# Kernel tuning notes

Hardware: AMD Instinct MI355X
Metric: run time of the kernel (lower is better)

Reference implementation:

```python
import jax, jax.numpy as jnp
import numpy as np

N_NODES = 40000
N_EDGES = 1280000
D_FEAT = 1024
HIDDEN = 64
N_CLASSES = 40


def gcn_conv(x, edge_index, W, b):
    # PyG GCNConv: linear transform, add self-loops, symmetric deg^{-1/2} normalization, scatter-add
    n = x.shape[0]
    h = x @ W  # [N, out]
    loop = jnp.arange(n, dtype=edge_index.dtype)
    row = jnp.concatenate([edge_index[0], loop])  # source
    col = jnp.concatenate([edge_index[1], loop])  # target
    deg = jax.ops.segment_sum(jnp.ones_like(col, dtype=x.dtype), col, num_segments=n)
    dinv = jnp.where(deg > 0, jax.lax.rsqrt(deg), 0.0).astype(x.dtype)
    norm = dinv[row] * dinv[col]  # [E+N]
    msg = h[row] * norm[:, None]
    out = jax.ops.segment_sum(msg, col, num_segments=n)
    return out + b


def setup_inputs() -> dict:
    key = jax.random.key(0)
    k1, k2, k3, k4 = jax.random.split(key, 4)
    x = jax.random.normal(k1, (N_NODES, D_FEAT), dtype=jnp.float32)
    edge_index = jax.random.randint(k2, (2, N_EDGES), 0, N_NODES, dtype=jnp.int32)
    W1 = jax.random.normal(k3, (D_FEAT, HIDDEN), dtype=jnp.float32) * (1.0 / np.sqrt(D_FEAT))
    b1 = jnp.zeros((HIDDEN,), dtype=jnp.float32)
    W2 = jax.random.normal(k4, (HIDDEN, N_CLASSES), dtype=jnp.float32) * (1.0 / np.sqrt(HIDDEN))
    b2 = jnp.zeros((N_CLASSES,), dtype=jnp.float32)
    return {"x": x, "edge_index": edge_index, "W1": W1, "b1": b1, "W2": W2, "b2": b2}


def reference(x, edge_index, W1, b1, W2, b2):
    h = gcn_conv(x, edge_index, W1, b1)
    h = jax.nn.relu(h)
    # F.dropout(training=False) -> identity in eval mode
    h = gcn_conv(h, edge_index, W2, b2)
    return jax.nn.log_softmax(h, axis=1)
```

## Files before the change

kernel.cpp:

```cpp
#include <hip/hip_runtime.h>
#include <hip/hip_bf16.h>
#include <math.h>

#define N_NODES 40000
#define N_EDGES 1280000
#define D_FEAT 1024
#define HIDDEN 64
#define N_CLASSES 40
#define NB 157
#define CHUNK 8192

typedef _Float16 f16x8 __attribute__((ext_vector_type(8)));
typedef _Float16 f16x2 __attribute__((ext_vector_type(2)));
typedef float f32x4 __attribute__((ext_vector_type(4)));


#define HIST_BLOCKS 313
#define CONV_BLOCKS 256

__global__ __launch_bounds__(256) void k_pre(const int* __restrict__ col,
                                             int* __restrict__ btot,
                                             const float* __restrict__ W,
                                             _Float16* __restrict__ Wt) {
    __shared__ int h[NB];
    int tid = threadIdx.x;
    if (blockIdx.x < HIST_BLOCKS) {
        if (tid < NB) h[tid] = 0;
        __syncthreads();
        int e0 = blockIdx.x * 4096;
        int e1 = min(e0 + 4096, N_EDGES);
        for (int e = e0 + tid; e < e1; e += 256)
            atomicAdd(&h[col[e] >> 8], 1);
        __syncthreads();
        if (tid < NB && h[tid]) atomicAdd(&btot[tid], h[tid]);
    } else {
        int i = (blockIdx.x - HIST_BLOCKS) * 256 + tid;
        int n = i & 63, k = i >> 6;
        Wt[n * D_FEAT + k] = (_Float16)W[k * HIDDEN + n];
    }
}


__global__ __launch_bounds__(256) void k_bucketscan(const int* __restrict__ btot,
                                                    int* __restrict__ bucketBase,
                                                    int* __restrict__ bucketCursor) {
    __shared__ int s[256];
    int tid = threadIdx.x;
    int v = (tid < NB) ? btot[tid] : 0;
    s[tid] = v;
    __syncthreads();
#pragma unroll
    for (int d = 1; d < 256; d <<= 1) {
        int t = (tid >= d) ? s[tid - d] : 0;
        __syncthreads();
        s[tid] += t;
        __syncthreads();
    }
    int excl = s[tid] - v;
    if (tid < NB) { bucketBase[tid] = excl; bucketCursor[tid] = excl; }
    if (tid == 0) bucketBase[NB] = N_EDGES;
}


__global__ __launch_bounds__(256) void k_binscatter(const int* __restrict__ row,
                                                    const int* __restrict__ col,
                                                    int* __restrict__ bucketCursor,
                                                    uint2* __restrict__ sedge) {
    __shared__ int hist[NB];
    __shared__ int chunkBase[NB];
    __shared__ int cur[NB];
    int tid = threadIdx.x;
    int e0 = blockIdx.x * CHUNK;
    int e1 = min(e0 + CHUNK, N_EDGES);
    if (tid < NB) { hist[tid] = 0; cur[tid] = 0; }
    __syncthreads();
    for (int e = e0 + tid; e < e1; e += 256)
        atomicAdd(&hist[col[e] >> 8], 1);
    __syncthreads();
    if (tid < NB)
        chunkBase[tid] = hist[tid] ? atomicAdd(&bucketCursor[tid], hist[tid]) : 0;
    __syncthreads();
    for (int e = e0 + tid; e < e1; e += 256) {
        int c = col[e];
        int b = c >> 8;
        int p = atomicAdd(&cur[b], 1);
        sedge[chunkBase[b] + p] = make_uint2((unsigned)row[e], (unsigned)c);
    }
}


__global__ __launch_bounds__(256) void k_bucketsort(const uint2* __restrict__ sedge,
                                                    const int* __restrict__ bucketBase,
                                                    int* __restrict__ off,
                                                    float* __restrict__ dinv,
                                                    int* __restrict__ sorted) {
    __shared__ int hist[256];
    __shared__ int s[256];
    __shared__ int cur[256];
    int tid = threadIdx.x;
    int b = blockIdx.x;
    int base = bucketBase[b], end = bucketBase[b + 1];
    int col0 = b << 8;
    int ncol = min(256, N_NODES - col0);
    hist[tid] = 0;
    __syncthreads();
    for (int i = base + tid; i < end; i += 256)
        atomicAdd(&hist[sedge[i].y & 255], 1);
    __syncthreads();
    int v = hist[tid];
    s[tid] = v;
    __syncthreads();
#pragma unroll
    for (int d = 1; d < 256; d <<= 1) {
        int t = (tid >= d) ? s[tid - d] : 0;
        __syncthreads();
        s[tid] += t;
        __syncthreads();
    }
    int excl = s[tid] - v;
    cur[tid] = excl;
    if (tid < ncol) {
        off[col0 + tid] = base + excl;
        dinv[col0 + tid] = rsqrtf((float)(v + 1));
    }
    if (b == NB - 1 && tid == 0) off[N_NODES] = N_EDGES;
    __syncthreads();
    for (int i = base + tid; i < end; i += 256) {
        uint2 e = sedge[i];
        int p = atomicAdd(&cur[e.y & 255], 1);
        sorted[base + p] = (int)e.x;
    }
}


#define LDA 72
#define LDB 72

__global__ __launch_bounds__(256) void k_gemm1(const float* __restrict__ X,
                                               const _Float16* __restrict__ Wt,
                                               const float* __restrict__ dinv,
                                               _Float16* __restrict__ out) {
    __shared__ _Float16 As[64 * LDA];
    __shared__ _Float16 Bs[64 * LDB];
    const int tid = threadIdx.x;
    const int wave = tid >> 6, lane = tid & 63;
    const int row0 = blockIdx.x * 64;
    const int m0 = wave * 16;
    const int lr = lane & 15, quad = lane >> 4;

    const int ar = tid >> 2;
    const int ak = (tid & 3) * 16;

    f32x4 acc0 = {0.f,0.f,0.f,0.f}, acc1 = {0.f,0.f,0.f,0.f};
    f32x4 acc2 = {0.f,0.f,0.f,0.f}, acc3 = {0.f,0.f,0.f,0.f};

    for (int k0 = 0; k0 < D_FEAT; k0 += 64) {
        const float* xp = &X[(row0 + ar) * D_FEAT + k0 + ak];
        float4 v0 = *(const float4*)(xp + 0);
        float4 v1 = *(const float4*)(xp + 4);
        float4 v2 = *(const float4*)(xp + 8);
        float4 v3 = *(const float4*)(xp + 12);
        f16x8 p0 = {(_Float16)v0.x,(_Float16)v0.y,(_Float16)v0.z,(_Float16)v0.w,
                    (_Float16)v1.x,(_Float16)v1.y,(_Float16)v1.z,(_Float16)v1.w};
        f16x8 p1 = {(_Float16)v2.x,(_Float16)v2.y,(_Float16)v2.z,(_Float16)v2.w,
                    (_Float16)v3.x,(_Float16)v3.y,(_Float16)v3.z,(_Float16)v3.w};
        *(f16x8*)&As[ar * LDA + ak]     = p0;
        *(f16x8*)&As[ar * LDA + ak + 8] = p1;
        const uint4* wp = (const uint4*)&Wt[ar * D_FEAT + k0 + ak];
        uint4 w0 = wp[0], w1 = wp[1];
        *(uint4*)&Bs[ar * LDB + ak]     = w0;
        *(uint4*)&Bs[ar * LDB + ak + 8] = w1;
        __syncthreads();
#pragma unroll
        for (int kk = 0; kk < 64; kk += 32) {
            f16x8 a  = *(f16x8*)&As[(m0 + lr) * LDA + kk + quad * 8];
            f16x8 b0 = *(f16x8*)&Bs[( 0 + lr) * LDB + kk + quad * 8];
            f16x8 b1 = *(f16x8*)&Bs[(16 + lr) * LDB + kk + quad * 8];
            f16x8 b2 = *(f16x8*)&Bs[(32 + lr) * LDB + kk + quad * 8];
            f16x8 b3 = *(f16x8*)&Bs[(48 + lr) * LDB + kk + quad * 8];
            acc0 = __builtin_amdgcn_mfma_f32_16x16x32_f16(a, b0, acc0, 0, 0, 0);
            acc1 = __builtin_amdgcn_mfma_f32_16x16x32_f16(a, b1, acc1, 0, 0, 0);
            acc2 = __builtin_amdgcn_mfma_f32_16x16x32_f16(a, b2, acc2, 0, 0, 0);
            acc3 = __builtin_amdgcn_mfma_f32_16x16x32_f16(a, b3, acc3, 0, 0, 0);
        }
        __syncthreads();
    }

#pragma unroll
    for (int r = 0; r < 4; ++r) {
        int m = row0 + m0 + quad * 4 + r;
        float dv = dinv[m];
        out[m * HIDDEN +  0 + lr] = (_Float16)(acc0[r] * dv);
        out[m * HIDDEN + 16 + lr] = (_Float16)(acc1[r] * dv);
        out[m * HIDDEN + 32 + lr] = (_Float16)(acc2[r] * dv);
        out[m * HIDDEN + 48 + lr] = (_Float16)(acc3[r] * dv);
    }
}


__global__ __launch_bounds__(256) void k_g1g2(const int* __restrict__ off,
                                              const int* __restrict__ sorted,
                                              const _Float16* __restrict__ hs,
                                              const float* __restrict__ dinv,
                                              const float* __restrict__ bias,
                                              const float* __restrict__ W2,
                                              _Float16* __restrict__ B3) {
    __shared__ float W2t[N_CLASSES][65];
    __shared__ float a1s[4][64];
    const int tid = threadIdx.x;
    const int wave = tid >> 6, lane = tid & 63;
    const int node = blockIdx.x * 4 + wave;

    for (int i = tid; i < HIDDEN * N_CLASSES; i += 256)
        W2t[i % N_CLASSES][i / N_CLASSES] = W2[i];

    int h = lane >> 5, fl = lane & 31;
    float ax = 0.f, ay = 0.f;
    if (h == 0) {
        f16x2 v = *(const f16x2*)&hs[node * HIDDEN + 2 * fl];
        ax = (float)v.x; ay = (float)v.y;
    }
    int beg = off[node], end = off[node + 1];
    int j = beg + h;
    for (; j + 6 < end; j += 8) {
        int s0 = sorted[j], s1 = sorted[j + 2], s2 = sorted[j + 4], s3 = sorted[j + 6];
        f16x2 v0 = *(const f16x2*)&hs[s0 * HIDDEN + 2 * fl];
        f16x2 v1 = *(const f16x2*)&hs[s1 * HIDDEN + 2 * fl];
        f16x2 v2 = *(const f16x2*)&hs[s2 * HIDDEN + 2 * fl];
        f16x2 v3 = *(const f16x2*)&hs[s3 * HIDDEN + 2 * fl];
        ax += (float)v0.x + (float)v1.x + (float)v2.x + (float)v3.x;
        ay += (float)v0.y + (float)v1.y + (float)v2.y + (float)v3.y;
    }
    for (; j < end; j += 2) {
        int s = sorted[j];
        f16x2 v = *(const f16x2*)&hs[s * HIDDEN + 2 * fl];
        ax += (float)v.x; ay += (float)v.y;
    }
    ax += __shfl_xor(ax, 32, 64);
    ay += __shfl_xor(ay, 32, 64);
    float dv = dinv[node];
    if (h == 0) {
        float2 o;
        o.x = fmaxf(fmaf(dv, ax, bias[2 * fl + 0]), 0.f);
        o.y = fmaxf(fmaf(dv, ay, bias[2 * fl + 1]), 0.f);
        *(float2*)&a1s[wave][2 * fl] = o;
    }
    __syncthreads();

    if (lane < N_CLASSES) {
        float acc = 0.f;
#pragma unroll
        for (int k = 0; k < HIDDEN; ++k)
            acc = fmaf(a1s[wave][k], W2t[lane][k], acc);
        B3[node * N_CLASSES + lane] = (_Float16)(acc * dv);
    }
}


__global__ __launch_bounds__(256) void k_gather2_lsm(const int* __restrict__ off,
                                                     const int* __restrict__ sorted,
                                                     const _Float16* __restrict__ hs,
                                                     const float* __restrict__ dinv,
                                                     const float* __restrict__ bias,
                                                     float* __restrict__ out) {
    int node = (blockIdx.x * 256 + threadIdx.x) >> 6;
    int lane = threadIdx.x & 63;
    if (node >= N_NODES) return;
    int h = lane >> 5, fl = lane & 31;
    bool act = fl < 20;
    float ax = 0.f, ay = 0.f;
    if (h == 0 && act) {
        f16x2 v = *(const f16x2*)&hs[node * N_CLASSES + 2 * fl];
        ax = (float)v.x; ay = (float)v.y;
    }
    int beg = off[node], end = off[node + 1];
    int j = beg + h;
    for (; j + 6 < end; j += 8) {
        int s0 = sorted[j], s1 = sorted[j + 2], s2 = sorted[j + 4], s3 = sorted[j + 6];
        if (act) {
            f16x2 v0 = *(const f16x2*)&hs[s0 * N_CLASSES + 2 * fl];
            f16x2 v1 = *(const f16x2*)&hs[s1 * N_CLASSES + 2 * fl];
            f16x2 v2 = *(const f16x2*)&hs[s2 * N_CLASSES + 2 * fl];
            f16x2 v3 = *(const f16x2*)&hs[s3 * N_CLASSES + 2 * fl];
            ax += (float)v0.x + (float)v1.x + (float)v2.x + (float)v3.x;
            ay += (float)v0.y + (float)v1.y + (float)v2.y + (float)v3.y;
        }
    }
    for (; j < end; j += 2) {
        int s = sorted[j];
        if (act) {
            f16x2 v = *(const f16x2*)&hs[s * N_CLASSES + 2 * fl];
            ax += (float)v.x; ay += (float)v.y;
        }
    }
    ax += __shfl_xor(ax, 32, 64);
    ay += __shfl_xor(ay, 32, 64);
    float dv = dinv[node];
    float zx = act ? fmaf(dv, ax, bias[2 * fl + 0]) : -INFINITY;
    float zy = act ? fmaf(dv, ay, bias[2 * fl + 1]) : -INFINITY;
    float m = fmaxf(zx, zy);
#pragma unroll
    for (int d = 16; d > 0; d >>= 1) m = fmaxf(m, __shfl_xor(m, d, 64));
    float ex = act ? (expf(zx - m) + expf(zy - m)) : 0.f;
#pragma unroll
    for (int d = 16; d > 0; d >>= 1) ex += __shfl_xor(ex, d, 64);
    float lse = m + logf(ex);
    if (h == 0 && act) {
        float2 o; o.x = zx - lse; o.y = zy - lse;
        *(float2*)&out[node * N_CLASSES + 2 * fl] = o;
    }
}


extern "C" void kernel_launch(void* const* d_in, const int* in_sizes, int n_in,
                              void* d_out, int out_size, void* d_ws, size_t ws_size,
                              hipStream_t stream) {
    const float* x  = (const float*)d_in[0];
    const int*   ei = (const int*)d_in[1];
    const float* W1 = (const float*)d_in[2];
    const float* b1 = (const float*)d_in[3];
    const float* W2 = (const float*)d_in[4];
    const float* b2 = (const float*)d_in[5];
    const int* row = ei;
    const int* col = ei + N_EDGES;

    char* ws = (char*)d_ws;
    int*      btot         = (int*)(ws + 0);
    int*      bucketBase   = (int*)(ws + 1024);
    int*      bucketCursor = (int*)(ws + 2048);
    int*      off          = (int*)(ws + 4096);
    float*    dinv         = (float*)(ws + 172032);
    uint2*    sedge        = (uint2*)(ws + 335872);
    int*      sorted       = (int*)(ws + 10575872);
    _Float16* W1t          = (_Float16*)(ws + 15695872);
    _Float16* B1           = (_Float16*)(ws + 15826944);
    _Float16* B3           = (_Float16*)(ws + 20946944);

    hipMemsetAsync(btot, 0, NB * sizeof(int), stream);
    k_pre<<<HIST_BLOCKS + CONV_BLOCKS, 256, 0, stream>>>(col, btot, W1, W1t);
    k_bucketscan<<<1, 256, 0, stream>>>(btot, bucketBase, bucketCursor);
    k_binscatter<<<(N_EDGES + CHUNK - 1) / CHUNK, 256, 0, stream>>>(row, col, bucketCursor, sedge);
    k_bucketsort<<<NB, 256, 0, stream>>>(sedge, bucketBase, off, dinv, sorted);

    k_gemm1<<<N_NODES / 64, 256, 0, stream>>>(x, W1t, dinv, B1);
    k_g1g2<<<N_NODES / 4, 256, 0, stream>>>(off, sorted, B1, dinv, b1, W2, B3);
    k_gather2_lsm<<<(N_NODES + 3) / 4, 256, 0, stream>>>(off, sorted, B3, dinv, b2, (float*)d_out);
}
```

Baseline: 409.8 us.

## Compress edge indices, stage binscatter in LDS, drop scan kernel, retile GEMM

Several changes land at once. The separate bucket-scan kernel is removed and each consumer recomputes the prefix sum. Binned edges are packed into 32-bit words and the sorted source list is stored as 16-bit indices, which cuts the bytes moved through sorting and gathering. Binscatter now sorts each chunk in LDS so its global writes are contiguous. The gathers load 64 neighbor indices per wave and broadcast them with shuffles, and GEMM1 uses 32-row tiles so it launches more blocks. The 16-bit index packing only works because node ids fit in 16 bits, and the redundant scans add some per-block work.

```diff
diff --git a/kernel.cpp b/kernel.cpp
--- a/kernel.cpp
+++ b/kernel.cpp
@@ -8,7 +8,7 @@
 #define HIDDEN 64
 #define N_CLASSES 40
 #define NB 157
-#define CHUNK 8192
+#define CHUNK 4096
 
 typedef _Float16 f16x8 __attribute__((ext_vector_type(8)));
 typedef _Float16 f16x2 __attribute__((ext_vector_type(2)));
@@ -41,84 +41,121 @@
 }
 
 
-__global__ __launch_bounds__(256) void k_bucketscan(const int* __restrict__ btot,
-                                                    int* __restrict__ bucketBase,
-                                                    int* __restrict__ bucketCursor) {
-    __shared__ int s[256];
-    int tid = threadIdx.x;
-    int v = (tid < NB) ? btot[tid] : 0;
-    s[tid] = v;
-    __syncthreads();
-#pragma unroll
-    for (int d = 1; d < 256; d <<= 1) {
-        int t = (tid >= d) ? s[tid - d] : 0;
-        __syncthreads();
-        s[tid] += t;
-        __syncthreads();
-    }
-    int excl = s[tid] - v;
-    if (tid < NB) { bucketBase[tid] = excl; bucketCursor[tid] = excl; }
-    if (tid == 0) bucketBase[NB] = N_EDGES;
-}
-
-
 __global__ __launch_bounds__(256) void k_binscatter(const int* __restrict__ row,
                                                     const int* __restrict__ col,
-                                                    int* __restrict__ bucketCursor,
-                                                    uint2* __restrict__ sedge) {
+                                                    const int* __restrict__ btot,
+                                                    int* __restrict__ gcur,
+                                                    unsigned* __restrict__ sedge) {
+    __shared__ unsigned stage[CHUNK];
+    __shared__ unsigned char bo[CHUNK];
+    __shared__ int sc[256];
+    __shared__ int bb[NB];
     __shared__ int hist[NB];
-    __shared__ int chunkBase[NB];
+    __shared__ int lo[NB];
     __shared__ int cur[NB];
-    int tid = threadIdx.x;
-    int e0 = blockIdx.x * CHUNK;
-    int e1 = min(e0 + CHUNK, N_EDGES);
+    __shared__ int dst[NB];
+    const int tid = threadIdx.x;
+    const int e0 = blockIdx.x * CHUNK;
+    const int nE = min(CHUNK, N_EDGES - e0);
+
     if (tid < NB) { hist[tid] = 0; cur[tid] = 0; }
-    __syncthreads();
-    for (int e = e0 + tid; e < e1; e += 256)
-        atomicAdd(&hist[col[e] >> 8], 1);
-    __syncthreads();
-    if (tid < NB)
-        chunkBase[tid] = hist[tid] ? atomicAdd(&bucketCursor[tid], hist[tid]) : 0;
-    __syncthreads();
-    for (int e = e0 + tid; e < e1; e += 256) {
-        int c = col[e];
-        int b = c >> 8;
-        int p = atomicAdd(&cur[b], 1);
-        sedge[chunkBase[b] + p] = make_uint2((unsigned)row[e], (unsigned)c);
-    }
-}
-
-
-__global__ __launch_bounds__(256) void k_bucketsort(const uint2* __restrict__ sedge,
-                                                    const int* __restrict__ bucketBase,
+    int bv = (tid < NB) ? btot[tid] : 0;
+    sc[tid] = bv;
+    __syncthreads();
+#pragma unroll
+    for (int d = 1; d < 256; d <<= 1) {
+        int t = (tid >= d) ? sc[tid - d] : 0;
+        __syncthreads();
+        sc[tid] += t;
+        __syncthreads();
+    }
+    if (tid < NB) bb[tid] = sc[tid] - bv;
+
+    int c[16];
+#pragma unroll
+    for (int t = 0; t < 16; ++t) {
+        int e = tid + t * 256;
+        c[t] = (e < nE) ? col[e0 + e] : -1;
+        if (e < nE) atomicAdd(&hist[c[t] >> 8], 1);
+    }
+    __syncthreads();
+
+    int hv = (tid < NB) ? hist[tid] : 0;
+    sc[tid] = hv;
+    __syncthreads();
+#pragma unroll
+    for (int d = 1; d < 256; d <<= 1) {
+        int t = (tid >= d) ? sc[tid - d] : 0;
+        __syncthreads();
+        sc[tid] += t;
+        __syncthreads();
+    }
+    if (tid < NB) {
+        int excl = sc[tid] - hv;
+        lo[tid] = excl;
+        int cp = hv ? atomicAdd(&gcur[tid], hv) : 0;
+        dst[tid] = bb[tid] + cp - excl;
+    }
+    __syncthreads();
+
+#pragma unroll
+    for (int t = 0; t < 16; ++t) {
+        int e = tid + t * 256;
+        if (e < nE) {
+            int b = c[t] >> 8;
+            int p = lo[b] + atomicAdd(&cur[b], 1);
+            stage[p] = ((unsigned)(c[t] & 255) << 16) | (unsigned)row[e0 + e];
+            bo[p] = (unsigned char)b;
+        }
+    }
+    __syncthreads();
+    for (int i = tid; i < nE; i += 256)
+        sedge[dst[bo[i]] + i] = stage[i];
+}
+
+
+__global__ __launch_bounds__(256) void k_bucketsort(const unsigned* __restrict__ sedge,
+                                                    const int* __restrict__ btot,
                                                     int* __restrict__ off,
                                                     float* __restrict__ dinv,
-                                                    int* __restrict__ sorted) {
+                                                    unsigned short* __restrict__ sorted) {
+    __shared__ int sc[256];
     __shared__ int hist[256];
-    __shared__ int s[256];
     __shared__ int cur[256];
-    int tid = threadIdx.x;
-    int b = blockIdx.x;
-    int base = bucketBase[b], end = bucketBase[b + 1];
+    const int tid = threadIdx.x;
+    const int b = blockIdx.x;
+    int bv = (tid < NB) ? btot[tid] : 0;
+    sc[tid] = bv;
+    hist[tid] = 0;
+    __syncthreads();
+#pragma unroll
+    for (int d = 1; d < 256; d <<= 1) {
+        int t = (tid >= d) ? sc[tid - d] : 0;
+        __syncthreads();
+        sc[tid] += t;
+        __syncthreads();
+    }
+    const int base = (b == 0) ? 0 : sc[b - 1];
+    const int end  = sc[b];
+    __syncthreads();
+
+    for (int i = base + tid; i < end; i += 256)
+        atomicAdd(&hist[sedge[i] >> 16], 1);
+    __syncthreads();
+    int v = hist[tid];
+    sc[tid] = v;
+    __syncthreads();
+#pragma unroll
+    for (int d = 1; d < 256; d <<= 1) {
+        int t = (tid >= d) ? sc[tid - d] : 0;
+        __syncthreads();
+        sc[tid] += t;
+        __syncthreads();
+    }
+    int excl = sc[tid] - v;
+    cur[tid] = excl;
     int col0 = b << 8;
     int ncol = min(256, N_NODES - col0);
-    hist[tid] = 0;
-    __syncthreads();
-    for (int i = base + tid; i < end; i += 256)
-        atomicAdd(&hist[sedge[i].y & 255], 1);
-    __syncthreads();
-    int v = hist[tid];
-    s[tid] = v;
-    __syncthreads();
-#pragma unroll
-    for (int d = 1; d < 256; d <<= 1) {
-        int t = (tid >= d) ? s[tid - d] : 0;
-        __syncthreads();
-        s[tid] += t;
-        __syncthreads();
-    }
-    int excl = s[tid] - v;
-    cur[tid] = excl;
     if (tid < ncol) {
         off[col0 + tid] = base + excl;
         dinv[col0 + tid] = rsqrtf((float)(v + 1));
@@ -126,9 +163,9 @@
     if (b == NB - 1 && tid == 0) off[N_NODES] = N_EDGES;
     __syncthreads();
     for (int i = base + tid; i < end; i += 256) {
-        uint2 e = sedge[i];
-        int p = atomicAdd(&cur[e.y & 255], 1);
-        sorted[base + p] = (int)e.x;
+        unsigned e = sedge[i];
+        int p = atomicAdd(&cur[e >> 16], 1);
+        sorted[base + p] = (unsigned short)e;
     }
 }
 
@@ -140,48 +177,40 @@
                                                const _Float16* __restrict__ Wt,
                                                const float* __restrict__ dinv,
                                                _Float16* __restrict__ out) {
-    __shared__ _Float16 As[64 * LDA];
+    __shared__ _Float16 As[32 * LDA];
     __shared__ _Float16 Bs[64 * LDB];
     const int tid = threadIdx.x;
     const int wave = tid >> 6, lane = tid & 63;
-    const int row0 = blockIdx.x * 64;
-    const int m0 = wave * 16;
+    const int row0 = blockIdx.x * 32;
+    const int m0 = (wave & 1) * 16, n0 = (wave >> 1) * 32;
     const int lr = lane & 15, quad = lane >> 4;
 
-    const int ar = tid >> 2;
-    const int ak = (tid & 3) * 16;
+    const int ar = tid >> 3;
+    const int ak = (tid & 7) * 8;
+    const int bn = tid >> 2;
+    const int bk = (tid & 3) * 16;
 
     f32x4 acc0 = {0.f,0.f,0.f,0.f}, acc1 = {0.f,0.f,0.f,0.f};
-    f32x4 acc2 = {0.f,0.f,0.f,0.f}, acc3 = {0.f,0.f,0.f,0.f};
 
     for (int k0 = 0; k0 < D_FEAT; k0 += 64) {
         const float* xp = &X[(row0 + ar) * D_FEAT + k0 + ak];
         float4 v0 = *(const float4*)(xp + 0);
         float4 v1 = *(const float4*)(xp + 4);
-        float4 v2 = *(const float4*)(xp + 8);
-        float4 v3 = *(const float4*)(xp + 12);
         f16x8 p0 = {(_Float16)v0.x,(_Float16)v0.y,(_Float16)v0.z,(_Float16)v0.w,
                     (_Float16)v1.x,(_Float16)v1.y,(_Float16)v1.z,(_Float16)v1.w};
-        f16x8 p1 = {(_Float16)v2.x,(_Float16)v2.y,(_Float16)v2.z,(_Float16)v2.w,
-                    (_Float16)v3.x,(_Float16)v3.y,(_Float16)v3.z,(_Float16)v3.w};
-        *(f16x8*)&As[ar * LDA + ak]     = p0;
-        *(f16x8*)&As[ar * LDA + ak + 8] = p1;
-        const uint4* wp = (const uint4*)&Wt[ar * D_FEAT + k0 + ak];
+        *(f16x8*)&As[ar * LDA + ak] = p0;
+        const uint4* wp = (const uint4*)&Wt[bn * D_FEAT + k0 + bk];
         uint4 w0 = wp[0], w1 = wp[1];
-        *(uint4*)&Bs[ar * LDB + ak]     = w0;
-        *(uint4*)&Bs[ar * LDB + ak + 8] = w1;
+        *(uint4*)&Bs[bn * LDB + bk]     = w0;
+        *(uint4*)&Bs[bn * LDB + bk + 8] = w1;
         __syncthreads();
 #pragma unroll
         for (int kk = 0; kk < 64; kk += 32) {
             f16x8 a  = *(f16x8*)&As[(m0 + lr) * LDA + kk + quad * 8];
-            f16x8 b0 = *(f16x8*)&Bs[( 0 + lr) * LDB + kk + quad * 8];
-            f16x8 b1 = *(f16x8*)&Bs[(16 + lr) * LDB + kk + quad * 8];
-            f16x8 b2 = *(f16x8*)&Bs[(32 + lr) * LDB + kk + quad * 8];
-            f16x8 b3 = *(f16x8*)&Bs[(48 + lr) * LDB + kk + quad * 8];
+            f16x8 b0 = *(f16x8*)&Bs[(n0 + lr) * LDB + kk + quad * 8];
+            f16x8 b1 = *(f16x8*)&Bs[(n0 + 16 + lr) * LDB + kk + quad * 8];
             acc0 = __builtin_amdgcn_mfma_f32_16x16x32_f16(a, b0, acc0, 0, 0, 0);
             acc1 = __builtin_amdgcn_mfma_f32_16x16x32_f16(a, b1, acc1, 0, 0, 0);
-            acc2 = __builtin_amdgcn_mfma_f32_16x16x32_f16(a, b2, acc2, 0, 0, 0);
-            acc3 = __builtin_amdgcn_mfma_f32_16x16x32_f16(a, b3, acc3, 0, 0, 0);
         }
         __syncthreads();
     }
@@ -190,16 +219,14 @@
     for (int r = 0; r < 4; ++r) {
         int m = row0 + m0 + quad * 4 + r;
         float dv = dinv[m];
-        out[m * HIDDEN +  0 + lr] = (_Float16)(acc0[r] * dv);
-        out[m * HIDDEN + 16 + lr] = (_Float16)(acc1[r] * dv);
-        out[m * HIDDEN + 32 + lr] = (_Float16)(acc2[r] * dv);
-        out[m * HIDDEN + 48 + lr] = (_Float16)(acc3[r] * dv);
+        out[m * HIDDEN + n0 + lr]      = (_Float16)(acc0[r] * dv);
+        out[m * HIDDEN + n0 + 16 + lr] = (_Float16)(acc1[r] * dv);
     }
 }
 
 
 __global__ __launch_bounds__(256) void k_g1g2(const int* __restrict__ off,
-                                              const int* __restrict__ sorted,
+                                              const unsigned short* __restrict__ sorted,
                                               const _Float16* __restrict__ hs,
                                               const float* __restrict__ dinv,
                                               const float* __restrict__ bias,
@@ -221,20 +248,27 @@
         ax = (float)v.x; ay = (float)v.y;
     }
     int beg = off[node], end = off[node + 1];
-    int j = beg + h;
-    for (; j + 6 < end; j += 8) {
-        int s0 = sorted[j], s1 = sorted[j + 2], s2 = sorted[j + 4], s3 = sorted[j + 6];
-        f16x2 v0 = *(const f16x2*)&hs[s0 * HIDDEN + 2 * fl];
-        f16x2 v1 = *(const f16x2*)&hs[s1 * HIDDEN + 2 * fl];
-        f16x2 v2 = *(const f16x2*)&hs[s2 * HIDDEN + 2 * fl];
-        f16x2 v3 = *(const f16x2*)&hs[s3 * HIDDEN + 2 * fl];
-        ax += (float)v0.x + (float)v1.x + (float)v2.x + (float)v3.x;
-        ay += (float)v0.y + (float)v1.y + (float)v2.y + (float)v3.y;
-    }
-    for (; j < end; j += 2) {
-        int s = sorted[j];
-        f16x2 v = *(const f16x2*)&hs[s * HIDDEN + 2 * fl];
-        ax += (float)v.x; ay += (float)v.y;
+    for (int base = beg; base < end; base += 64) {
+        int m = end - base; if (m > 64) m = 64;
+        int vidx = (lane < m) ? (int)sorted[base + lane] : 0;
+        int i = h;
+        for (; i + 6 < m; i += 8) {
+            int s0 = __shfl(vidx, i,     64);
+            int s1 = __shfl(vidx, i + 2, 64);
+            int s2 = __shfl(vidx, i + 4, 64);
+            int s3 = __shfl(vidx, i + 6, 64);
+            f16x2 v0 = *(const f16x2*)&hs[s0 * HIDDEN + 2 * fl];
+            f16x2 v1 = *(const f16x2*)&hs[s1 * HIDDEN + 2 * fl];
+            f16x2 v2 = *(const f16x2*)&hs[s2 * HIDDEN + 2 * fl];
+            f16x2 v3 = *(const f16x2*)&hs[s3 * HIDDEN + 2 * fl];
+            ax += (float)v0.x + (float)v1.x + (float)v2.x + (float)v3.x;
+            ay += (float)v0.y + (float)v1.y + (float)v2.y + (float)v3.y;
+        }
+        for (; i < m; i += 2) {
+            int s = __shfl(vidx, i, 64);
+            f16x2 v = *(const f16x2*)&hs[s * HIDDEN + 2 * fl];
+            ax += (float)v.x; ay += (float)v.y;
+        }
     }
     ax += __shfl_xor(ax, 32, 64);
     ay += __shfl_xor(ay, 32, 64);
@@ -258,7 +292,7 @@
 
 
 __global__ __launch_bounds__(256) void k_gather2_lsm(const int* __restrict__ off,
-                                                     const int* __restrict__ sorted,
+                                                     const unsigned short* __restrict__ sorted,
                                                      const _Float16* __restrict__ hs,
                                                      const float* __restrict__ dinv,
                                                      const float* __restrict__ bias,
@@ -274,23 +308,30 @@
         ax = (float)v.x; ay = (float)v.y;
     }
     int beg = off[node], end = off[node + 1];
-    int j = beg + h;
-    for (; j + 6 < end; j += 8) {
-        int s0 = sorted[j], s1 = sorted[j + 2], s2 = sorted[j + 4], s3 = sorted[j + 6];
-        if (act) {
-            f16x2 v0 = *(const f16x2*)&hs[s0 * N_CLASSES + 2 * fl];
-            f16x2 v1 = *(const f16x2*)&hs[s1 * N_CLASSES + 2 * fl];
-            f16x2 v2 = *(const f16x2*)&hs[s2 * N_CLASSES + 2 * fl];
-            f16x2 v3 = *(const f16x2*)&hs[s3 * N_CLASSES + 2 * fl];
-            ax += (float)v0.x + (float)v1.x + (float)v2.x + (float)v3.x;
-            ay += (float)v0.y + (float)v1.y + (float)v2.y + (float)v3.y;
-        }
-    }
-    for (; j < end; j += 2) {
-        int s = sorted[j];
-        if (act) {
-            f16x2 v = *(const f16x2*)&hs[s * N_CLASSES + 2 * fl];
-            ax += (float)v.x; ay += (float)v.y;
+    for (int base = beg; base < end; base += 64) {
+        int m = end - base; if (m > 64) m = 64;
+        int vidx = (lane < m) ? (int)sorted[base + lane] : 0;
+        int i = h;
+        for (; i + 6 < m; i += 8) {
+            int s0 = __shfl(vidx, i,     64);
+            int s1 = __shfl(vidx, i + 2, 64);
+            int s2 = __shfl(vidx, i + 4, 64);
+            int s3 = __shfl(vidx, i + 6, 64);
+            if (act) {
+                f16x2 v0 = *(const f16x2*)&hs[s0 * N_CLASSES + 2 * fl];
+                f16x2 v1 = *(const f16x2*)&hs[s1 * N_CLASSES + 2 * fl];
+                f16x2 v2 = *(const f16x2*)&hs[s2 * N_CLASSES + 2 * fl];
+                f16x2 v3 = *(const f16x2*)&hs[s3 * N_CLASSES + 2 * fl];
+                ax += (float)v0.x + (float)v1.x + (float)v2.x + (float)v3.x;
+                ay += (float)v0.y + (float)v1.y + (float)v2.y + (float)v3.y;
+            }
+        }
+        for (; i < m; i += 2) {
+            int s = __shfl(vidx, i, 64);
+            if (act) {
+                f16x2 v = *(const f16x2*)&hs[s * N_CLASSES + 2 * fl];
+                ax += (float)v.x; ay += (float)v.y;
+            }
         }
     }
     ax += __shfl_xor(ax, 32, 64);
@@ -325,24 +366,22 @@
     const int* col = ei + N_EDGES;
 
     char* ws = (char*)d_ws;
-    int*      btot         = (int*)(ws + 0);
-    int*      bucketBase   = (int*)(ws + 1024);
-    int*      bucketCursor = (int*)(ws + 2048);
-    int*      off          = (int*)(ws + 4096);
-    float*    dinv         = (float*)(ws + 172032);
-    uint2*    sedge        = (uint2*)(ws + 335872);
-    int*      sorted       = (int*)(ws + 10575872);
-    _Float16* W1t          = (_Float16*)(ws + 15695872);
-    _Float16* B1           = (_Float16*)(ws + 15826944);
-    _Float16* B3           = (_Float16*)(ws + 20946944);
-
-    hipMemsetAsync(btot, 0, NB * sizeof(int), stream);
+    int*            btot   = (int*)(ws + 0);
+    int*            gcur   = (int*)(ws + 1024);
+    int*            off    = (int*)(ws + 4096);
+    float*          dinv   = (float*)(ws + 167936);
+    unsigned*       sedge  = (unsigned*)(ws + 335872);
+    unsigned short* sorted = (unsigned short*)(ws + 5455872);
+    _Float16*       W1t    = (_Float16*)(ws + 8015872);
+    _Float16*       B1     = (_Float16*)(ws + 8146944);
+    _Float16*       B3     = (_Float16*)(ws + 13266944);
+
+    hipMemsetAsync(btot, 0, 2048, stream);
     k_pre<<<HIST_BLOCKS + CONV_BLOCKS, 256, 0, stream>>>(col, btot, W1, W1t);
-    k_bucketscan<<<1, 256, 0, stream>>>(btot, bucketBase, bucketCursor);
-    k_binscatter<<<(N_EDGES + CHUNK - 1) / CHUNK, 256, 0, stream>>>(row, col, bucketCursor, sedge);
-    k_bucketsort<<<NB, 256, 0, stream>>>(sedge, bucketBase, off, dinv, sorted);
-
-    k_gemm1<<<N_NODES / 64, 256, 0, stream>>>(x, W1t, dinv, B1);
+    k_binscatter<<<(N_EDGES + CHUNK - 1) / CHUNK, 256, 0, stream>>>(row, col, btot, gcur, sedge);
+    k_bucketsort<<<NB, 256, 0, stream>>>(sedge, btot, off, dinv, sorted);
+
+    k_gemm1<<<N_NODES / 32, 256, 0, stream>>>(x, W1t, dinv, B1);
     k_g1g2<<<N_NODES / 4, 256, 0, stream>>>(off, sorted, B1, dinv, b1, W2, B3);
     k_gather2_lsm<<<(N_NODES + 3) / 4, 256, 0, stream>>>(off, sorted, B3, dinv, b2, (float*)d_out);
 }
```

Measured after the change: 385.1 us. 6.0% less time.
